# Optimization experiments

Hardware: AMD Instinct MI355X
Metric: run time of the kernel (lower is better)

## Reference

```python
import jax, jax.numpy as jnp
import numpy as np

TEMPERATURE = 0.1

def _l2norm(x):
    return x / jnp.linalg.norm(x, axis=-1, keepdims=True)

def setup_inputs() -> dict:
    key = jax.random.key(0)
    k1, k2, k3 = jax.random.split(key, 3)
    N_AUG, B, F, Q = 2, 256, 128, 65536
    V = _l2norm(jax.random.normal(k1, (N_AUG, B, F), dtype=jnp.float32))
    L = _l2norm(jax.random.normal(k2, (B, F), dtype=jnp.float32))
    queue = _l2norm(jax.random.normal(k3, (Q, F), dtype=jnp.float32))
    return {"V": V, "L": L, "queue": queue}

def reference(V, L, queue):
    # V: (J, B, F), L: (B, F), queue: (Q, F)
    J, B, F = V.shape
    inv_t = 1.0 / TEMPERATURE
    # pos[j, b] = V[j, b] . L[b] / T  (diagonal batch pairings)
    pos = jnp.einsum('jbf,bf->jb', V, L) * inv_t                 # (J, B)
    # qlog[j, b, q] = V[j, b] . queue[q] / T
    qlog = jnp.einsum('jbf,qf->jbq', V, queue) * inv_t           # (J, B, Q)
    # Original: denom[j,b] = log( sum_i exp(pos[j,i]) + sum_q exp(qlog[j,b,q]) )
    # == logsumexp over the concatenation of pos[j,:] and qlog[j,b,:].
    bat = jnp.broadcast_to(pos[:, None, :], (J, B, B))           # (J, B, B)
    combined = jnp.concatenate([bat, qlog], axis=-1)             # (J, B, B+Q)
    denom = jax.nn.logsumexp(combined, axis=-1)                  # (J, B)
    # loss = -(1/B) * sum_{b} sum_{j} (pos[j,b] - denom[j,b])
    loss = -jnp.sum(pos - denom) / B
    return loss
```

## Files before the change

kernel.cpp:

```cpp
#include <hip/hip_runtime.h>


typedef float  float4v __attribute__((ext_vector_type(4)));
typedef short  short8  __attribute__((ext_vector_type(8)));

#define AS1 __attribute__((address_space(1)))
#define AS3 __attribute__((address_space(3)))

__device__ __forceinline__ unsigned short f2bf(float f) {
    union { float f; unsigned u; } v; v.f = f;
    unsigned r = v.u + 0x7FFFu + ((v.u >> 16) & 1u);
    return (unsigned short)(r >> 16);
}


__global__ __launch_bounds__(256) void convert_prep_kernel(
        const float* __restrict__ V, const float* __restrict__ L,
        const float* __restrict__ Qf,
        unsigned short* __restrict__ qbf, unsigned short* __restrict__ abf,
        float* __restrict__ pos, float* __restrict__ Sq) {
    const int tid = threadIdx.x;
    const int gt  = blockIdx.x * 256 + tid;
    const float4* q4 = (const float4*)Qf;
    uint2* qo = (uint2*)qbf;
    #pragma unroll
    for (int i = 0; i < 4; ++i) {
        const int g = i * 524288 + gt;
        const float4 q = q4[g];
        uint2 p;
        p.x = (unsigned)f2bf(q.x) | ((unsigned)f2bf(q.y) << 16);
        p.y = (unsigned)f2bf(q.z) | ((unsigned)f2bf(q.w) << 16);
        qo[g] = p;
    }
    if (blockIdx.x < 64) {
        const float4 v = ((const float4*)V)[gt];
        uint2 p;
        p.x = (unsigned)f2bf(v.x) | ((unsigned)f2bf(v.y) << 16);
        p.y = (unsigned)f2bf(v.z) | ((unsigned)f2bf(v.w) << 16);
        ((uint2*)abf)[gt] = p;
    } else if (blockIdx.x < 128) {
        const int blk  = blockIdx.x - 64;
        if (tid < 8) Sq[blk * 8 + tid] = 0.0f;
        const int w    = tid >> 6;
        const int lane = tid & 63;
        #pragma unroll
        for (int i = 0; i < 2; ++i) {
            const int r = blk * 8 + w * 2 + i;
            const int b = r & 255;
            const float2 v = *reinterpret_cast<const float2*>(V + r * 128 + lane * 2);
            const float2 l = *reinterpret_cast<const float2*>(L + b * 128 + lane * 2);
            float p = v.x * l.x + v.y * l.y;
            #pragma unroll
            for (int off = 32; off; off >>= 1) p += __shfl_xor(p, off);
            if (lane == 0) pos[r] = 10.0f * p;
        }
    }
}

__global__ __launch_bounds__(256, 1) void gemm_exp_kernel(
        const unsigned short* __restrict__ abf,
        const unsigned short* __restrict__ qbf,
        float* __restrict__ Sq) {
    __shared__ unsigned short As[256 * 128];
    __shared__ unsigned short Bs[2][64 * 128];
    __shared__ float rowsum[256];

    const int tid  = threadIdx.x;
    const int bid  = blockIdx.x;
    const int mt   = bid >> 7;
    const int ng   = bid & 127;
    const int m0   = mt * 256;
    const int nb   = ng * 512;

    const int w    = tid >> 6;
    const int lane = tid & 63;
    const int quad = lane >> 4;
    const int l16  = lane & 15;
    const int wrow = w * 64;

    #pragma unroll
    for (int r = 0; r < 16; ++r) {
        const int slot = r * 256 + w * 64 + lane;
        const int row  = slot >> 4;
        const int cc   = slot & 15;
        const int c    = cc ^ (row & 15);
        const unsigned short* src = abf + (m0 + row) * 128 + c * 8;
        __builtin_amdgcn_global_load_lds((AS1 void*)src,
            (AS3 void*)&As[(r * 256 + w * 64) * 8], 16, 0, 0);
    }

    auto issueB = [&](int t) {
        unsigned short* buf = &Bs[t & 1][0];
        const unsigned short* base = qbf + (nb + t * 64) * 128;
        #pragma unroll
        for (int r = 0; r < 4; ++r) {
            const int slot = r * 256 + w * 64 + lane;
            const int row  = slot >> 4;
            const int cc   = slot & 15;
            const int c    = cc ^ (row & 15);
            __builtin_amdgcn_global_load_lds((AS1 void*)(base + row * 128 + c * 8),
                (AS3 void*)&buf[(r * 256 + w * 64) * 8], 16, 0, 0);
        }
    };
    issueB(0);
    issueB(1);

    float rs[4][4];
    #pragma unroll
    for (int mi = 0; mi < 4; ++mi)
        #pragma unroll
        for (int r = 0; r < 4; ++r) rs[mi][r] = 0.0f;

    #pragma unroll
    for (int t = 0; t < 8; ++t) {
        if (t < 7) __builtin_amdgcn_s_waitcnt(0x0F74);
        else       __builtin_amdgcn_s_waitcnt(0x0F70);
        __builtin_amdgcn_s_barrier();
        const unsigned short* buf = &Bs[t & 1][0];

        float4v acc[4][4];
        #pragma unroll
        for (int mi = 0; mi < 4; ++mi)
            #pragma unroll
            for (int ni = 0; ni < 4; ++ni)
                acc[mi][ni] = (float4v){0.f, 0.f, 0.f, 0.f};

        #pragma unroll
        for (int kk = 0; kk < 4; ++kk) {
            const int c = kk * 4 + quad;
            short8 a[4], b[4];
            #pragma unroll
            for (int mi = 0; mi < 4; ++mi) {
                const int row = wrow + mi * 16 + l16;
                a[mi] = *(const short8*)&As[row * 128 + ((c ^ (row & 15)) << 3)];
            }
            #pragma unroll
            for (int ni = 0; ni < 4; ++ni) {
                const int row = ni * 16 + l16;
                b[ni] = *(const short8*)&buf[row * 128 + ((c ^ (row & 15)) << 3)];
            }
            #pragma unroll
            for (int mi = 0; mi < 4; ++mi)
                #pragma unroll
                for (int ni = 0; ni < 4; ++ni)
                    acc[mi][ni] = __builtin_amdgcn_mfma_f32_16x16x32_bf16(a[mi], b[ni], acc[mi][ni], 0, 0, 0);
        }

        #pragma unroll
        for (int mi = 0; mi < 4; ++mi)
            #pragma unroll
            for (int ni = 0; ni < 4; ++ni)
                #pragma unroll
                for (int r = 0; r < 4; ++r)
                    rs[mi][r] += exp2f(acc[mi][ni][r] * 14.426950408889634f);

        if (t + 2 < 8) {
            __builtin_amdgcn_s_barrier();
            issueB(t + 2);
        }
    }

    #pragma unroll
    for (int mi = 0; mi < 4; ++mi)
        #pragma unroll
        for (int r = 0; r < 4; ++r) {
            float v = rs[mi][r];
            v += __shfl_xor(v, 1);
            v += __shfl_xor(v, 2);
            v += __shfl_xor(v, 4);
            v += __shfl_xor(v, 8);
            if (l16 == 0) rowsum[wrow + mi * 16 + quad * 4 + r] = v;
        }
    __syncthreads();
    atomicAdd(&Sq[m0 + tid], rowsum[tid]);
}


__global__ void prep_kernel(const float* __restrict__ V,
                            const float* __restrict__ L,
                            float* __restrict__ pos,
                            float* __restrict__ Sq) {
    const int blk  = blockIdx.x;
    const int tid  = threadIdx.x;
    if (tid < 8) Sq[blk * 8 + tid] = 0.0f;
    const int w    = tid >> 6;
    const int lane = tid & 63;
    #pragma unroll
    for (int i = 0; i < 2; ++i) {
        const int r = blk * 8 + w * 2 + i;
        const int b = r & 255;
        const float2 v = *reinterpret_cast<const float2*>(V + r * 128 + lane * 2);
        const float2 l = *reinterpret_cast<const float2*>(L + b * 128 + lane * 2);
        float p = v.x * l.x + v.y * l.y;
        #pragma unroll
        for (int off = 32; off; off >>= 1) p += __shfl_xor(p, off);
        if (lane == 0) pos[r] = 10.0f * p;
    }
}

__global__ __launch_bounds__(256) void gemm_exp_fallback(
        const float* __restrict__ V,
        const float* __restrict__ Q,
        float* __restrict__ Sq) {
    __shared__ unsigned short As[128 * 128];
    __shared__ unsigned short Bs[128 * 128];
    const int tid = threadIdx.x;
    const int m0  = blockIdx.y * 128;
    const int n0  = blockIdx.x * 128;
    #pragma unroll
    for (int i = 0; i < 16; ++i) {
        const int idx = i * 256 + tid;
        const int row = idx >> 5;
        const int c4  = idx & 31;
        const float4 a = *reinterpret_cast<const float4*>(V + (m0 + row) * 128 + c4 * 4);
        const float4 b = *reinterpret_cast<const float4*>(Q + (n0 + row) * 128 + c4 * 4);
        const int chunk = ((c4 >> 1) ^ (row & 15));
        const int off   = row * 128 + (chunk << 3) + ((c4 & 1) << 2);
        const uint2 pa = make_uint2((unsigned)f2bf(a.x) | ((unsigned)f2bf(a.y) << 16),
                                    (unsigned)f2bf(a.z) | ((unsigned)f2bf(a.w) << 16));
        const uint2 pb = make_uint2((unsigned)f2bf(b.x) | ((unsigned)f2bf(b.y) << 16),
                                    (unsigned)f2bf(b.z) | ((unsigned)f2bf(b.w) << 16));
        *reinterpret_cast<uint2*>(&As[off]) = pa;
        *reinterpret_cast<uint2*>(&Bs[off]) = pb;
    }
    __syncthreads();
    const int w    = tid >> 6;
    const int lane = tid & 63;
    const int quad = lane >> 4;
    const int l16  = lane & 15;
    const int wrow = (w >> 1) * 64;
    const int wcol = (w & 1) * 64;
    float4v acc[4][4];
    #pragma unroll
    for (int mi = 0; mi < 4; ++mi)
        #pragma unroll
        for (int ni = 0; ni < 4; ++ni)
            acc[mi][ni] = (float4v){0.f, 0.f, 0.f, 0.f};
    #pragma unroll
    for (int kk = 0; kk < 4; ++kk) {
        const int kchunk = kk * 4 + quad;
        short8 a[4], b[4];
        #pragma unroll
        for (int mi = 0; mi < 4; ++mi) {
            const int row = wrow + mi * 16 + l16;
            a[mi] = *reinterpret_cast<const short8*>(&As[row * 128 + ((kchunk ^ (row & 15)) << 3)]);
        }
        #pragma unroll
        for (int ni = 0; ni < 4; ++ni) {
            const int row = wcol + ni * 16 + l16;
            b[ni] = *reinterpret_cast<const short8*>(&Bs[row * 128 + ((kchunk ^ (row & 15)) << 3)]);
        }
        #pragma unroll
        for (int mi = 0; mi < 4; ++mi)
            #pragma unroll
            for (int ni = 0; ni < 4; ++ni)
                acc[mi][ni] = __builtin_amdgcn_mfma_f32_16x16x32_bf16(a[mi], b[ni], acc[mi][ni], 0, 0, 0);
    }
    __syncthreads();
    float* rowsum = reinterpret_cast<float*>(As);
    #pragma unroll
    for (int mi = 0; mi < 4; ++mi) {
        float rsv[4] = {0.f, 0.f, 0.f, 0.f};
        #pragma unroll
        for (int ni = 0; ni < 4; ++ni)
            #pragma unroll
            for (int r = 0; r < 4; ++r)
                rsv[r] += __expf(10.0f * acc[mi][ni][r]);
        #pragma unroll
        for (int r = 0; r < 4; ++r) {
            float vsum = rsv[r];
            vsum += __shfl_xor(vsum, 1);
            vsum += __shfl_xor(vsum, 2);
            vsum += __shfl_xor(vsum, 4);
            vsum += __shfl_xor(vsum, 8);
            if (l16 == 0)
                rowsum[(w & 1) * 128 + wrow + mi * 16 + quad * 4 + r] = vsum;
        }
    }
    __syncthreads();
    if (tid < 128)
        atomicAdd(&Sq[m0 + tid], rowsum[tid] + rowsum[128 + tid]);
}


__global__ void finalize_kernel(const float* __restrict__ pos,
                                const float* __restrict__ Sq,
                                float* __restrict__ out) {
    __shared__ float wsum[8];
    __shared__ float Sp[2];
    const int tid  = threadIdx.x;
    const int w    = tid >> 6;
    const int lane = tid & 63;
    const float p = pos[tid];
    float e = __expf(p);
    #pragma unroll
    for (int off = 32; off; off >>= 1) e += __shfl_xor(e, off);
    if (lane == 0) wsum[w] = e;
    __syncthreads();
    if (tid == 0) {
        Sp[0] = wsum[0] + wsum[1] + wsum[2] + wsum[3];
        Sp[1] = wsum[4] + wsum[5] + wsum[6] + wsum[7];
    }
    __syncthreads();
    const int j = tid >> 8;
    float contrib = p - __logf(Sp[j] + Sq[tid]);
    #pragma unroll
    for (int off = 32; off; off >>= 1) contrib += __shfl_xor(contrib, off);
    if (lane == 0) wsum[w] = contrib;
    __syncthreads();
    if (tid == 0) {
        float tot = 0.f;
        #pragma unroll
        for (int i = 0; i < 8; ++i) tot += wsum[i];
        out[0] = -tot / 256.0f;
    }
}


extern "C" void kernel_launch(void* const* d_in, const int* in_sizes, int n_in,
                              void* d_out, int out_size, void* d_ws, size_t ws_size,
                              hipStream_t stream) {
    const float* V     = (const float*)d_in[0];
    const float* L     = (const float*)d_in[1];
    const float* queue = (const float*)d_in[2];
    float* out = (float*)d_out;

    const size_t need = (size_t)65536 * 128 * 2 + (size_t)512 * 128 * 2 + 1024 * 4;
    if (ws_size >= need) {
        unsigned short* qbf = (unsigned short*)d_ws;
        unsigned short* abf = qbf + (size_t)65536 * 128;
        float* pos = (float*)(abf + 512 * 128);
        float* Sq  = pos + 512;
        convert_prep_kernel<<<2048, 256, 0, stream>>>(V, L, queue, qbf, abf, pos, Sq);
        gemm_exp_kernel<<<256, 256, 0, stream>>>(abf, qbf, Sq);
        finalize_kernel<<<1, 512, 0, stream>>>(pos, Sq, out);
    } else {
        float* pos = (float*)d_ws;
        float* Sq  = pos + 512;
        prep_kernel<<<64, 256, 0, stream>>>(V, L, pos, Sq);
        dim3 grid(512, 4);
        gemm_exp_fallback<<<grid, 256, 0, stream>>>(V, queue, Sq);
        finalize_kernel<<<1, 512, 0, stream>>>(pos, Sq, out);
    }
}
```

Baseline: 115.4 us.

## Keep A tile in registers and double grid to raise occupancy

Removes the 64KB shared-memory A tile and instead loads each wave's A fragments straight from global into registers once, reused across all N tiles. Each block now covers 256 queue columns instead of 512, so the grid doubles to 512 blocks, and launch bounds allow two blocks per CU. The goal is higher occupancy and more blocks to hide the B-tile load and exp latency, at the cost of extra register pressure (64 VGPRs for A) and twice as many A loads and atomics across blocks.

```diff
diff --git a/kernel.cpp b/kernel.cpp
--- a/kernel.cpp
+++ b/kernel.cpp
@@ -57,20 +57,19 @@
     }
 }
 
-__global__ __launch_bounds__(256, 1) void gemm_exp_kernel(
+__global__ __launch_bounds__(256, 2) void gemm_exp_kernel(
         const unsigned short* __restrict__ abf,
         const unsigned short* __restrict__ qbf,
         float* __restrict__ Sq) {
-    __shared__ unsigned short As[256 * 128];
     __shared__ unsigned short Bs[2][64 * 128];
     __shared__ float rowsum[256];
 
     const int tid  = threadIdx.x;
     const int bid  = blockIdx.x;
-    const int mt   = bid >> 7;
-    const int ng   = bid & 127;
+    const int mt   = bid >> 8;
+    const int ng   = bid & 255;
     const int m0   = mt * 256;
-    const int nb   = ng * 512;
+    const int nb   = ng * 256;
 
     const int w    = tid >> 6;
     const int lane = tid & 63;
@@ -78,16 +77,13 @@
     const int l16  = lane & 15;
     const int wrow = w * 64;
 
-    #pragma unroll
-    for (int r = 0; r < 16; ++r) {
-        const int slot = r * 256 + w * 64 + lane;
-        const int row  = slot >> 4;
-        const int cc   = slot & 15;
-        const int c    = cc ^ (row & 15);
-        const unsigned short* src = abf + (m0 + row) * 128 + c * 8;
-        __builtin_amdgcn_global_load_lds((AS1 void*)src,
-            (AS3 void*)&As[(r * 256 + w * 64) * 8], 16, 0, 0);
-    }
+    short8 a[4][4];
+    #pragma unroll
+    for (int mi = 0; mi < 4; ++mi)
+        #pragma unroll
+        for (int kk = 0; kk < 4; ++kk)
+            a[mi][kk] = *(const short8*)&abf[(m0 + wrow + mi * 16 + l16) * 128
+                                             + (kk * 4 + quad) * 8];
 
     auto issueB = [&](int t) {
         unsigned short* buf = &Bs[t & 1][0];
@@ -96,8 +92,7 @@
         for (int r = 0; r < 4; ++r) {
             const int slot = r * 256 + w * 64 + lane;
             const int row  = slot >> 4;
-            const int cc   = slot & 15;
-            const int c    = cc ^ (row & 15);
+            const int c    = (slot & 15) ^ (row & 15);
             __builtin_amdgcn_global_load_lds((AS1 void*)(base + row * 128 + c * 8),
                 (AS3 void*)&buf[(r * 256 + w * 64) * 8], 16, 0, 0);
         }
@@ -111,9 +106,9 @@
         #pragma unroll
         for (int r = 0; r < 4; ++r) rs[mi][r] = 0.0f;
 
-    #pragma unroll
-    for (int t = 0; t < 8; ++t) {
-        if (t < 7) __builtin_amdgcn_s_waitcnt(0x0F74);
+    #pragma unroll 1
+    for (int t = 0; t < 4; ++t) {
+        if (t < 3) __builtin_amdgcn_s_waitcnt(0x0F74);
         else       __builtin_amdgcn_s_waitcnt(0x0F70);
         __builtin_amdgcn_s_barrier();
         const unsigned short* buf = &Bs[t & 1][0];
@@ -128,12 +123,7 @@
         #pragma unroll
         for (int kk = 0; kk < 4; ++kk) {
             const int c = kk * 4 + quad;
-            short8 a[4], b[4];
-            #pragma unroll
-            for (int mi = 0; mi < 4; ++mi) {
-                const int row = wrow + mi * 16 + l16;
-                a[mi] = *(const short8*)&As[row * 128 + ((c ^ (row & 15)) << 3)];
-            }
+            short8 b[4];
             #pragma unroll
             for (int ni = 0; ni < 4; ++ni) {
                 const int row = ni * 16 + l16;
@@ -143,7 +133,8 @@
             for (int mi = 0; mi < 4; ++mi)
                 #pragma unroll
                 for (int ni = 0; ni < 4; ++ni)
-                    acc[mi][ni] = __builtin_amdgcn_mfma_f32_16x16x32_bf16(a[mi], b[ni], acc[mi][ni], 0, 0, 0);
+                    acc[mi][ni] = __builtin_amdgcn_mfma_f32_16x16x32_bf16(
+                        a[mi][kk], b[ni], acc[mi][ni], 0, 0, 0);
         }
 
         #pragma unroll
@@ -154,7 +145,7 @@
                 for (int r = 0; r < 4; ++r)
                     rs[mi][r] += exp2f(acc[mi][ni][r] * 14.426950408889634f);
 
-        if (t + 2 < 8) {
+        if (t < 2) {
             __builtin_amdgcn_s_barrier();
             issueB(t + 2);
         }
@@ -332,7 +323,7 @@
         float* pos = (float*)(abf + 512 * 128);
         float* Sq  = pos + 512;
         convert_prep_kernel<<<2048, 256, 0, stream>>>(V, L, queue, qbf, abf, pos, Sq);
-        gemm_exp_kernel<<<256, 256, 0, stream>>>(abf, qbf, Sq);
+        gemm_exp_kernel<<<512, 256, 0, stream>>>(abf, qbf, Sq);
         finalize_kernel<<<1, 512, 0, stream>>>(pos, Sq, out);
     } else {
         float* pos = (float*)d_ws;
```

New measurement: 106.8 us. -7.4%, faster.
